# Kernel tuning notes

Measured on AMD Instinct MI355X. Metric: run time of the kernel, lower is better.

The kernel has to match this reference:

```python
import math
import jax, jax.numpy as jnp
import numpy as np

jax.config.update("jax_enable_x64", True)  # exact int64 hash arithmetic like torch

L = 16
F = 2
T = 2 ** 18
NMIN = 16
NMAX = 2 ** 17
SMOOTHSTEP = False
_b = math.exp((math.log(NMAX) - math.log(NMIN)) / (L - 1))
NS = [int(math.floor(NMIN * _b ** l)) for l in range(L)]
PI2 = 2654435761
B = 2 ** 21


def setup_inputs() -> dict:
    key = jax.random.key(0)
    k1, k2 = jax.random.split(key)
    xy = jax.random.uniform(k1, (B, 2), dtype=jnp.float32)
    tables = jax.random.uniform(k2, (L, T, F), dtype=jnp.float32,
                                minval=-1e-4, maxval=1e-4)
    return {"xy": xy, "tables": tables}


def _encode(xy, tables):
    xy = jnp.clip(xy, 0.0, 1.0)
    feats = []
    for l in range(L):
        Nl = NS[l]
        table = tables[l]                      # (T, F)
        p = xy * Nl                            # (B, 2)
        p0 = jnp.floor(p).astype(jnp.int64)
        p1 = jnp.minimum(p0 + 1, Nl)
        w = p - p0.astype(p.dtype)
        if SMOOTHSTEP:
            w = w * w * (3.0 - 2.0 * w)
        x0, y0 = p0[:, 0], p0[:, 1]
        x1, y1 = p1[:, 0], p1[:, 1]
        if (Nl + 1) * (Nl + 1) <= T:
            def idx(xi, yi, Nl=Nl):
                return xi * (Nl + 1) + yi
        else:
            def idx(xi, yi):
                h = xi ^ (yi * PI2)
                return jnp.remainder(h, T)
        f00 = table[idx(x0, y0)]
        f10 = table[idx(x1, y0)]
        f01 = table[idx(x0, y1)]
        f11 = table[idx(x1, y1)]
        wx, wy = w[:, 0:1], w[:, 1:2]
        f0 = f00 * (1 - wx) + f10 * wx
        f1 = f01 * (1 - wx) + f11 * wx
        feats.append(f0 * (1 - wy) + f1 * wy)  # (B, F)
    return jnp.concatenate(feats, axis=1)      # (B, L*F)


def reference(xy, tables):
    return _encode(xy, tables)
```

## Files before the change

kernel.cpp:

```cpp
#include <hip/hip_runtime.h>
#include <math.h>
#include <stdint.h>

#define LVLS 16
#define TSZ (1 << 18)
#define TMASK (TSZ - 1)
#define PI2 2654435761u

struct NsParams { int ns[LVLS]; };

__global__ __launch_bounds__(256, 4) void hash_enc_kernel(
    const float* __restrict__ xy,
    const float* __restrict__ tables,
    float* __restrict__ out,
    int B, NsParams prm)
{
    __shared__ float smem[32 * 257];
    const int tid = threadIdx.x;
    const int i = blockIdx.x * 256 + tid;
    const int iclamp = i < B ? i : (B - 1);

    float2 q = reinterpret_cast<const float2*>(xy)[iclamp];
    float x = fminf(fmaxf(q.x, 0.0f), 1.0f);
    float y = fminf(fmaxf(q.y, 0.0f), 1.0f);

    float acc[2 * LVLS];

    #pragma unroll
    for (int l = 0; l < LVLS; ++l) {
        const int Nl = prm.ns[l];
        const float fN = (float)Nl;
        float px = x * fN, py = y * fN;
        float fx0 = floorf(px), fy0 = floorf(py);
        int x0 = (int)fx0, y0 = (int)fy0;
        int x1 = min(x0 + 1, Nl), y1 = min(y0 + 1, Nl);
        float wx = px - fx0, wy = py - fy0;

        const float2* tb = reinterpret_cast<const float2*>(tables) + (size_t)l * TSZ;

        uint32_t i00, i10, i01, i11;
        if ((long long)(Nl + 1) * (long long)(Nl + 1) <= (long long)TSZ) {
            uint32_t s = (uint32_t)(Nl + 1);
            i00 = (uint32_t)x0 * s + (uint32_t)y0;
            i10 = (uint32_t)x1 * s + (uint32_t)y0;
            i01 = (uint32_t)x0 * s + (uint32_t)y1;
            i11 = (uint32_t)x1 * s + (uint32_t)y1;
        } else {
            uint32_t hy0 = (uint32_t)y0 * PI2;
            uint32_t hy1 = (uint32_t)y1 * PI2;
            i00 = ((uint32_t)x0 ^ hy0) & TMASK;
            i10 = ((uint32_t)x1 ^ hy0) & TMASK;
            i01 = ((uint32_t)x0 ^ hy1) & TMASK;
            i11 = ((uint32_t)x1 ^ hy1) & TMASK;
        }

        float2 f00 = tb[i00];
        float2 f10 = tb[i10];
        float2 f01 = tb[i01];
        float2 f11 = tb[i11];

        float omwx = 1.0f - wx, omwy = 1.0f - wy;
        float f0a = f00.x * omwx + f10.x * wx;
        float f0b = f00.y * omwx + f10.y * wx;
        float f1a = f01.x * omwx + f11.x * wx;
        float f1b = f01.y * omwx + f11.y * wx;
        acc[2 * l]     = f0a * omwy + f1a * wy;
        acc[2 * l + 1] = f0b * omwy + f1b * wy;
    }

    #pragma unroll
    for (int c = 0; c < 32; ++c)
        smem[c * 257 + tid] = (i < B) ? acc[c] : 0.0f;
    __syncthreads();

    float4* out4 = reinterpret_cast<float4*>(out) + (size_t)blockIdx.x * 2048;
    const size_t out4_total = (size_t)B * 8;
    const int a = tid & 7, b = tid >> 3;
    #pragma unroll
    for (int j = 0; j < 8; ++j) {
        size_t gidx = (size_t)blockIdx.x * 2048 + j * 256 + tid;
        if (gidx < out4_total) {
            float4 v;
            v.x = smem[(4 * a + 0) * 257 + 32 * j + b];
            v.y = smem[(4 * a + 1) * 257 + 32 * j + b];
            v.z = smem[(4 * a + 2) * 257 + 32 * j + b];
            v.w = smem[(4 * a + 3) * 257 + 32 * j + b];
            out4[j * 256 + tid] = v;
        }
    }
}

extern "C" void kernel_launch(void* const* d_in, const int* in_sizes, int n_in,
                              void* d_out, int out_size, void* d_ws, size_t ws_size,
                              hipStream_t stream) {
    const float* xy     = (const float*)d_in[0];
    const float* tables = (const float*)d_in[1];
    float* out = (float*)d_out;
    const int B = in_sizes[0] / 2;

    NsParams prm;
    const double bb = exp((log(131072.0) - log(16.0)) / 15.0);
    for (int l = 0; l < LVLS; ++l)
        prm.ns[l] = (int)floor(16.0 * pow(bb, (double)l));

    const int grid = (B + 255) / 256;
    hipLaunchKernelGGL(hash_enc_kernel, dim3(grid), dim3(256), 0, stream,
                       xy, tables, out, B, prm);
}
```

Before: 1.050 ms.

## Shrink LDS transpose buffer with chunked staging to raise occupancy, add nontemporal stores

The output transpose now goes through LDS in four 64-point chunks, with a barrier before and after each, so the shared buffer drops from about 32 KB to about 9 KB. Launch bounds are raised to 8 waves-per-EU to allow more resident blocks for hiding gather latency. Output stores use nontemporal hints so they do not pollute the cache holding the hash tables. In exchange it adds seven extra block barriers, and the tighter launch bounds may cause register spills.

```diff
diff --git a/kernel.cpp b/kernel.cpp
--- a/kernel.cpp
+++ b/kernel.cpp
@@ -7,15 +7,17 @@
 #define TMASK (TSZ - 1)
 #define PI2 2654435761u
 
+typedef float f32x4 __attribute__((ext_vector_type(4)));
+
 struct NsParams { int ns[LVLS]; };
 
-__global__ __launch_bounds__(256, 4) void hash_enc_kernel(
+__global__ __launch_bounds__(256, 8) void hash_enc_kernel(
     const float* __restrict__ xy,
     const float* __restrict__ tables,
     float* __restrict__ out,
     int B, NsParams prm)
 {
-    __shared__ float smem[32 * 257];
+    __shared__ float smem[32 * 69];
     const int tid = threadIdx.x;
     const int i = blockIdx.x * 256 + tid;
     const int iclamp = i < B ? i : (B - 1);
@@ -68,25 +70,31 @@
         acc[2 * l + 1] = f0b * omwy + f1b * wy;
     }
 
-    #pragma unroll
-    for (int c = 0; c < 32; ++c)
-        smem[c * 257 + tid] = (i < B) ? acc[c] : 0.0f;
-    __syncthreads();
-
-    float4* out4 = reinterpret_cast<float4*>(out) + (size_t)blockIdx.x * 2048;
+    f32x4* out4 = reinterpret_cast<f32x4*>(out);
     const size_t out4_total = (size_t)B * 8;
-    const int a = tid & 7, b = tid >> 3;
-    #pragma unroll
-    for (int j = 0; j < 8; ++j) {
-        size_t gidx = (size_t)blockIdx.x * 2048 + j * 256 + tid;
-        if (gidx < out4_total) {
-            float4 v;
-            v.x = smem[(4 * a + 0) * 257 + 32 * j + b];
-            v.y = smem[(4 * a + 1) * 257 + 32 * j + b];
-            v.z = smem[(4 * a + 2) * 257 + 32 * j + b];
-            v.w = smem[(4 * a + 3) * 257 + 32 * j + b];
-            out4[j * 256 + tid] = v;
+    #pragma unroll 1
+    for (int ch = 0; ch < 4; ++ch) {
+        const int p64 = tid - (ch << 6);
+        if ((unsigned)p64 < 64u) {
+            #pragma unroll
+            for (int c = 0; c < 32; ++c)
+                smem[c * 69 + p64] = (i < B) ? acc[c] : 0.0f;
         }
+        __syncthreads();
+        #pragma unroll
+        for (int r = 0; r < 2; ++r) {
+            const int f = tid + (r << 8);
+            const int pp = f >> 3, k = f & 7;
+            f32x4 v;
+            v.x = smem[(4 * k + 0) * 69 + pp];
+            v.y = smem[(4 * k + 1) * 69 + pp];
+            v.z = smem[(4 * k + 2) * 69 + pp];
+            v.w = smem[(4 * k + 3) * 69 + pp];
+            size_t g = (size_t)blockIdx.x * 2048 + (size_t)(ch * 512 + f);
+            if (g < out4_total)
+                __builtin_nontemporal_store(v, &out4[g]);
+        }
+        __syncthreads();
     }
 }
 
```

After: 1.281 ms. +22.0%, slower.
